# Kernel optimization log

Measured on AMD Instinct MI355X. Metric: run time of the kernel, lower is better.

The kernel has to match this reference:

```python
import jax, jax.numpy as jnp
import numpy as np

N_FFT = 1024
HOP = 256
BATCH = 16
SAMPLES = 262144


def hann_window(n):
    # torch.hann_window default (periodic=True): 0.5 * (1 - cos(2*pi*k/n))
    k = jnp.arange(n, dtype=jnp.float32)
    return 0.5 - 0.5 * jnp.cos(2.0 * jnp.pi * k / n)


def setup_inputs() -> dict:
    key = jax.random.key(0)
    x = jax.random.normal(key, (BATCH, SAMPLES), dtype=jnp.float32)
    window = hann_window(N_FFT)  # (n_fft,)
    return {"x": x, "window": window}


def reference(x, window):
    # Faithful STFT.forward: pad -> frame (identity-kernel conv1d == gather) ->
    # window -> rfft along the frame axis; norm=None.
    pad = N_FFT - HOP
    pad_left = pad // 2
    xp = jnp.pad(x, ((0, 0), (pad_left, pad - pad_left)))
    n_frames = (xp.shape[1] - N_FFT) // HOP + 1
    # gather-based framing, equivalent to conv1d with eye(n_fft) kernel, stride=hop
    idx = jnp.arange(n_frames)[:, None] * HOP + jnp.arange(N_FFT)[None, :]  # (frames, n_fft)
    frames = xp[:, idx]                       # (B, frames, n_fft)
    frames = frames * window[None, None, :]   # windowing
    spec = jnp.fft.rfft(frames, axis=-1)      # (B, frames, n_bins)
    real = jnp.transpose(spec.real, (0, 2, 1))  # (B, n_bins, frames)
    imag = jnp.transpose(spec.imag, (0, 2, 1))
    return real, imag
```

## Files before the change

kernel.cpp:

```cpp
#include <hip/hip_runtime.h>

#define HOP      256
#define SAMPLES  262144
#define NBINS    513
#define NFRAMES  1024
#define FPB      16

__device__ __forceinline__ float2 cmul(float2 a, float2 b) {
  return make_float2(a.x * b.x - a.y * b.y, a.x * b.y + a.y * b.x);
}
__device__ __forceinline__ float2 lds_ld(const float2* p, int bo) {
  return *(const float2*)((const char*)p + bo);
}
__device__ __forceinline__ void lds_st(float2* p, int bo, float2 v) {
  *(float2*)((char*)p + bo) = v;
}
__device__ __forceinline__ int swz(int c) {
  int H = c >> 6, M = (c >> 3) & 7, L = c & 7;
  return (H << 6) | ((M ^ (H & 1)) << 3) | (L ^ M);
}

__device__ __forceinline__ void fft8(float2 v[8]) {
  const float R = 0.70710678118654752440f;
  float2 s0 = make_float2(v[0].x + v[4].x, v[0].y + v[4].y);
  float2 d0 = make_float2(v[0].x - v[4].x, v[0].y - v[4].y);
  float2 s1 = make_float2(v[1].x + v[5].x, v[1].y + v[5].y);
  float2 d1 = make_float2(v[1].x - v[5].x, v[1].y - v[5].y);
  float2 s2 = make_float2(v[2].x + v[6].x, v[2].y + v[6].y);
  float2 d2 = make_float2(v[2].x - v[6].x, v[2].y - v[6].y);
  float2 s3 = make_float2(v[3].x + v[7].x, v[3].y + v[7].y);
  float2 d3 = make_float2(v[3].x - v[7].x, v[3].y - v[7].y);
  float2 e1 = make_float2(R * (d1.x + d1.y), R * (d1.y - d1.x));
  float2 e2 = make_float2(d2.y, -d2.x);
  float2 e3 = make_float2(R * (d3.y - d3.x), R * (-d3.x - d3.y));
  float2 p0 = make_float2(s0.x + s2.x, s0.y + s2.y);
  float2 q0 = make_float2(s0.x - s2.x, s0.y - s2.y);
  float2 p1 = make_float2(s1.x + s3.x, s1.y + s3.y);
  float2 q1 = make_float2(s1.x - s3.x, s1.y - s3.y);
  float2 q1t = make_float2(q1.y, -q1.x);
  float2 p2 = make_float2(d0.x + e2.x, d0.y + e2.y);
  float2 q2 = make_float2(d0.x - e2.x, d0.y - e2.y);
  float2 p3 = make_float2(e1.x + e3.x, e1.y + e3.y);
  float2 q3 = make_float2(e1.x - e3.x, e1.y - e3.y);
  float2 q3t = make_float2(q3.y, -q3.x);
  v[0] = make_float2(p0.x + p1.x, p0.y + p1.y);
  v[4] = make_float2(p0.x - p1.x, p0.y - p1.y);
  v[2] = make_float2(q0.x + q1t.x, q0.y + q1t.y);
  v[6] = make_float2(q0.x - q1t.x, q0.y - q1t.y);
  v[1] = make_float2(p2.x + p3.x, p2.y + p3.y);
  v[5] = make_float2(p2.x - p3.x, p2.y - p3.y);
  v[3] = make_float2(q2.x + q3t.x, q2.y + q3t.y);
  v[7] = make_float2(q2.x - q3t.x, q2.y - q3t.y);
}

#define UNPK(ZP, KEY, SK, SM, TW, R1, I1, R2, I2) {                  \
    float2 Zk = lds_ld(ZP, ((SK) ^ (KEY)) << 3);                     \
    float2 Zm = lds_ld(ZP, ((SM) ^ (KEY)) << 3);                     \
    float xer  = 0.5f * (Zk.x + Zm.x);                               \
    float xei  = 0.5f * (Zk.y - Zm.y);                               \
    float xo_r = 0.5f * (Zk.y + Zm.y);                               \
    float xo_i = -0.5f * (Zk.x - Zm.x);                              \
    float ur = (TW).x * xo_r - (TW).y * xo_i;                        \
    float ui = (TW).x * xo_i + (TW).y * xo_r;                        \
    R1 = xer + ur; I1 = xei + ui; R2 = xer - ur; I2 = ui - xei; }

__global__ __launch_bounds__(1024, 8)
void stft_kernel(const float* __restrict__ x, const float* __restrict__ win,
                 float* __restrict__ out) {
  __shared__ float2 z[FPB * 512];
  const int t  = threadIdx.x;
  const int b  = blockIdx.x >> 6;
  const int f0 = (blockIdx.x & 63) * FPB;

  {
    const int w = t >> 6;
    const int u = t & 63;
    const int g = u >> 3, m2l = u & 7;
    float2* zf = z + (w << 9);

    const int A0    = (g << 3) | (m2l ^ g);
    const int B1w_e = (A0 ^ w) << 3;
    const int B1w_o = B1w_e ^ 64;
    const int C1    = (g << 6) | ((g & 1) << 3) | m2l;
    const int B1r   = (C1 ^ w) << 3;
    const int D0    = (g << 6) | ((m2l ^ (g & 1)) << 3) | m2l;
    const int B2r   = (D0 ^ w) << 3;
    const int F0    = (m2l << 3) | (g ^ m2l);
    const int B3_e  = (F0 ^ w) << 3;
    const int B3_o  = B3_e ^ 64;

    const float* xb = x + (size_t)b * SAMPLES;
    const int fr   = f0 + w;
    const int base = fr * HOP - 384;
    float2 r[8];
    if (f0 != 0 && f0 != (NFRAMES - FPB)) {
      const float2* xc = (const float2*)(xb + base);
      const float2* wc = (const float2*)win;
#pragma unroll
      for (int n1 = 0; n1 < 8; ++n1) {
        float2 xv = xc[(n1 << 6) + u];
        float2 wv = wc[(n1 << 6) + u];
        r[n1] = make_float2(xv.x * wv.x, xv.y * wv.y);
      }
    } else {
#pragma unroll
      for (int n1 = 0; n1 < 8; ++n1) {
        int s = (n1 << 7) + 2 * u;
        int idx = base + s;
        float2 xv = make_float2(0.f, 0.f);
        if (idx >= 0 && idx < SAMPLES) xv = *(const float2*)(xb + idx);
        float2 wv = *(const float2*)(win + s);
        r[n1] = make_float2(xv.x * wv.x, xv.y * wv.y);
      }
    }

    fft8(r);
    float sn, cs;
    __sincosf((float)u * (-6.28318530717958647693f / 512.f), &sn, &cs);
    {
      float2 w1 = make_float2(cs, sn);
      float2 w2 = cmul(w1, w1);
      float2 w3 = cmul(w2, w1);
      float2 w4 = cmul(w2, w2);
      r[1] = cmul(r[1], w1);
      r[2] = cmul(r[2], w2);
      r[3] = cmul(r[3], w3);
      r[4] = cmul(r[4], w4);
      r[5] = cmul(r[5], cmul(w4, w1));
      r[6] = cmul(r[6], cmul(w4, w2));
      r[7] = cmul(r[7], cmul(w4, w3));
    }
    lds_st(zf, B1w_e,        r[0]);
    lds_st(zf, B1w_o +  512, r[1]);
    lds_st(zf, B1w_e + 1024, r[2]);
    lds_st(zf, B1w_o + 1536, r[3]);
    lds_st(zf, B1w_e + 2048, r[4]);
    lds_st(zf, B1w_o + 2560, r[5]);
    lds_st(zf, B1w_e + 3072, r[6]);
    lds_st(zf, B1w_o + 3584, r[7]);

    float2 y[8];
#pragma unroll
    for (int m1 = 0; m1 < 8; ++m1) y[m1] = lds_ld(zf, B1r ^ (72 * m1));

    fft8(y);
    __sincosf((float)m2l * (-6.28318530717958647693f / 64.f), &sn, &cs);
    {
      float2 w1 = make_float2(cs, sn);
      float2 w2 = cmul(w1, w1);
      float2 w3 = cmul(w2, w1);
      float2 w4 = cmul(w2, w2);
      y[1] = cmul(y[1], w1);
      y[2] = cmul(y[2], w2);
      y[3] = cmul(y[3], w3);
      y[4] = cmul(y[4], w4);
      y[5] = cmul(y[5], cmul(w4, w1));
      y[6] = cmul(y[6], cmul(w4, w2));
      y[7] = cmul(y[7], cmul(w4, w3));
    }
#pragma unroll
    for (int j1 = 0; j1 < 8; ++j1) lds_st(zf, B1r ^ (72 * j1), y[j1]);

    float2 h[8];
#pragma unroll
    for (int m = 0; m < 8; ++m) h[m] = lds_ld(zf, B2r ^ (m << 3));

    fft8(h);
    lds_st(zf, B3_e,        h[0]);
    lds_st(zf, B3_o +  512, h[1]);
    lds_st(zf, B3_e + 1024, h[2]);
    lds_st(zf, B3_o + 1536, h[3]);
    lds_st(zf, B3_e + 2048, h[4]);
    lds_st(zf, B3_o + 2560, h[5]);
    lds_st(zf, B3_e + 3072, h[6]);
    lds_st(zf, B3_o + 3584, h[7]);
  }
  __syncthreads();

  {
    const int f2i = t & 7;
    const int q   = t >> 3;
    const int f   = f2i << 1;
    const int fr  = f0 + f;
    const float2* zp0 = z + (f << 9);
    const float2* zp1 = z + ((f + 1) << 9);

    const int sk0 = swz(q);
    const int sm0 = swz((512 - q) & 511);
    const int sk1 = sk0 + 128;
    const int sm1 = (q == 0) ? 384 : (sm0 - 128);

    float sn, cs;
    __sincosf((float)q * (-6.28318530717958647693f / 1024.f), &sn, &cs);
    const float2 tw0 = make_float2(cs, sn);
    const float2 tw1 = cmul(tw0, make_float2(0.70710678118654752440f,
                                             -0.70710678118654752440f));
    float* out_r = out;
    float* out_i = out + (size_t)16 * NBINS * NFRAMES;
    const size_t o1 = ((size_t)b * NBINS + q) * NFRAMES + fr;
    const size_t o2 = ((size_t)b * NBINS + (512 - q)) * NFRAMES + fr;
    const size_t STP = (size_t)128 * NFRAMES;

    {
      float r1a, i1a, r2a, i2a, r1b, i1b, r2b, i2b;
      UNPK(zp0, f,     sk0, sm0, tw0, r1a, i1a, r2a, i2a)
      UNPK(zp1, f + 1, sk0, sm0, tw0, r1b, i1b, r2b, i2b)
      *(float2*)(out_r + o1) = make_float2(r1a, r1b);
      *(float2*)(out_i + o1) = make_float2(i1a, i1b);
      *(float2*)(out_r + o2) = make_float2(r2a, r2b);
      *(float2*)(out_i + o2) = make_float2(i2a, i2b);
    }
    {
      float r1a, i1a, r2a, i2a, r1b, i1b, r2b, i2b;
      UNPK(zp0, f,     sk1, sm1, tw1, r1a, i1a, r2a, i2a)
      UNPK(zp1, f + 1, sk1, sm1, tw1, r1b, i1b, r2b, i2b)
      *(float2*)(out_r + o1 + STP) = make_float2(r1a, r1b);
      *(float2*)(out_i + o1 + STP) = make_float2(i1a, i1b);
      *(float2*)(out_r + o2 - STP) = make_float2(r2a, r2b);
      *(float2*)(out_i + o2 - STP) = make_float2(i2a, i2b);
    }
    if (q == 0) {
      float2 Za = lds_ld(zp0, (256 ^ f) << 3);
      float2 Zb = lds_ld(zp1, (256 ^ (f + 1)) << 3);
      const size_t o6 = ((size_t)b * NBINS + 256) * NFRAMES + fr;
      *(float2*)(out_r + o6) = make_float2(Za.x, Zb.x);
      *(float2*)(out_i + o6) = make_float2(-Za.y, -Zb.y);
    }
  }
}

extern "C" void kernel_launch(void* const* d_in, const int* in_sizes, int n_in,
                              void* d_out, int out_size, void* d_ws, size_t ws_size,
                              hipStream_t stream) {
  const float* x = (const float*)d_in[0];
  const float* w = (const float*)d_in[1];
  float* out = (float*)d_out;
  (void)in_sizes; (void)n_in; (void)out_size; (void)d_ws; (void)ws_size;
  stft_kernel<<<dim3(1024), dim3(1024), 0, stream>>>(x, w, out);
}
```

Before: 24.41 us.

## Halve block size and process two frames per thread in STFT kernel

Each block now runs 512 threads instead of 1024, and every 64-thread group computes two FFT frames (w and w+8) with interleaved stages. The twiddle factors and window loads are shared across both frames, and the unpack phase loops over two quarter-ranges per thread. The aim is more instruction-level parallelism and less repeated setup per frame. In exchange, register pressure rises and there are fewer threads to hide latency.

```diff
diff --git a/kernel.cpp b/kernel.cpp
--- a/kernel.cpp
+++ b/kernel.cpp
@@ -53,6 +53,48 @@
   v[7] = make_float2(q2.x - q3t.x, q2.y - q3t.y);
 }
 
+#define FFT_S1(R, ZF, E1, O1) {                                          \
+    fft8(R);                                                             \
+    R[1] = cmul(R[1], s1w1);  R[2] = cmul(R[2], s1w2);                   \
+    R[3] = cmul(R[3], s1w3);  R[4] = cmul(R[4], s1w4);                   \
+    R[5] = cmul(R[5], s1w5);  R[6] = cmul(R[6], s1w6);                   \
+    R[7] = cmul(R[7], s1w7);                                             \
+    lds_st(ZF, (E1),        R[0]);                                       \
+    lds_st(ZF, (O1) +  512, R[1]);                                       \
+    lds_st(ZF, (E1) + 1024, R[2]);                                       \
+    lds_st(ZF, (O1) + 1536, R[3]);                                       \
+    lds_st(ZF, (E1) + 2048, R[4]);                                       \
+    lds_st(ZF, (O1) + 2560, R[5]);                                       \
+    lds_st(ZF, (E1) + 3072, R[6]);                                       \
+    lds_st(ZF, (O1) + 3584, R[7]);                                       \
+  }
+
+#define FFT_S2(Y, ZF, BR) {                                              \
+    _Pragma("unroll")                                                    \
+    for (int m1 = 0; m1 < 8; ++m1) Y[m1] = lds_ld(ZF, (BR) ^ (72 * m1)); \
+    fft8(Y);                                                             \
+    Y[1] = cmul(Y[1], s2w1);  Y[2] = cmul(Y[2], s2w2);                   \
+    Y[3] = cmul(Y[3], s2w3);  Y[4] = cmul(Y[4], s2w4);                   \
+    Y[5] = cmul(Y[5], s2w5);  Y[6] = cmul(Y[6], s2w6);                   \
+    Y[7] = cmul(Y[7], s2w7);                                             \
+    _Pragma("unroll")                                                    \
+    for (int j1 = 0; j1 < 8; ++j1) lds_st(ZF, (BR) ^ (72 * j1), Y[j1]);  \
+  }
+
+#define FFT_S3(H, ZF, B2, E3, O3) {                                      \
+    _Pragma("unroll")                                                    \
+    for (int m = 0; m < 8; ++m) H[m] = lds_ld(ZF, (B2) ^ (m << 3));      \
+    fft8(H);                                                             \
+    lds_st(ZF, (E3),        H[0]);                                       \
+    lds_st(ZF, (O3) +  512, H[1]);                                       \
+    lds_st(ZF, (E3) + 1024, H[2]);                                       \
+    lds_st(ZF, (O3) + 1536, H[3]);                                       \
+    lds_st(ZF, (E3) + 2048, H[4]);                                       \
+    lds_st(ZF, (O3) + 2560, H[5]);                                       \
+    lds_st(ZF, (E3) + 3072, H[6]);                                       \
+    lds_st(ZF, (O3) + 3584, H[7]);                                       \
+  }
+
 #define UNPK(ZP, KEY, SK, SM, TW, R1, I1, R2, I2) {                  \
     float2 Zk = lds_ld(ZP, ((SK) ^ (KEY)) << 3);                     \
     float2 Zm = lds_ld(ZP, ((SM) ^ (KEY)) << 3);                     \
@@ -64,7 +106,7 @@
     float ui = (TW).x * xo_i + (TW).y * xo_r;                        \
     R1 = xer + ur; I1 = xei + ui; R2 = xer - ur; I2 = ui - xei; }
 
-__global__ __launch_bounds__(1024, 8)
+__global__ __launch_bounds__(512, 4)
 void stft_kernel(const float* __restrict__ x, const float* __restrict__ win,
                  float* __restrict__ out) {
   __shared__ float2 z[FPB * 512];
@@ -76,7 +118,8 @@
     const int w = t >> 6;
     const int u = t & 63;
     const int g = u >> 3, m2l = u & 7;
-    float2* zf = z + (w << 9);
+    float2* zfA = z + (w << 9);
+    float2* zfB = z + ((w + 8) << 9);
 
     const int A0    = (g << 3) | (m2l ^ g);
     const int B1w_e = (A0 ^ w) << 3;
@@ -90,90 +133,74 @@
     const int B3_o  = B3_e ^ 64;
 
     const float* xb = x + (size_t)b * SAMPLES;
-    const int fr   = f0 + w;
-    const int base = fr * HOP - 384;
-    float2 r[8];
-    if (f0 != 0 && f0 != (NFRAMES - FPB)) {
-      const float2* xc = (const float2*)(xb + base);
-      const float2* wc = (const float2*)win;
+    const int baseA = (f0 + w) * HOP - 384;
+    const int baseB = baseA + 8 * HOP;
+    const float2* wc = (const float2*)win;
+    float2 ra[8], rb[8];
+    if (f0 != 0) {
+      const float2* xc = (const float2*)(xb + baseA);
+#pragma unroll
+      for (int n1 = 0; n1 < 8; ++n1) ra[n1] = xc[(n1 << 6) + u];
+    } else {
 #pragma unroll
       for (int n1 = 0; n1 < 8; ++n1) {
-        float2 xv = xc[(n1 << 6) + u];
-        float2 wv = wc[(n1 << 6) + u];
-        r[n1] = make_float2(xv.x * wv.x, xv.y * wv.y);
-      }
+        int idx = baseA + (n1 << 7) + 2 * u;
+        ra[n1] = make_float2(0.f, 0.f);
+        if (idx >= 0) ra[n1] = *(const float2*)(xb + idx);
+      }
+    }
+    if (f0 != (NFRAMES - FPB)) {
+      const float2* xc = (const float2*)(xb + baseB);
+#pragma unroll
+      for (int n1 = 0; n1 < 8; ++n1) rb[n1] = xc[(n1 << 6) + u];
     } else {
 #pragma unroll
       for (int n1 = 0; n1 < 8; ++n1) {
-        int s = (n1 << 7) + 2 * u;
-        int idx = base + s;
-        float2 xv = make_float2(0.f, 0.f);
-        if (idx >= 0 && idx < SAMPLES) xv = *(const float2*)(xb + idx);
-        float2 wv = *(const float2*)(win + s);
-        r[n1] = make_float2(xv.x * wv.x, xv.y * wv.y);
-      }
-    }
-
-    fft8(r);
+        int idx = baseB + (n1 << 7) + 2 * u;
+        rb[n1] = make_float2(0.f, 0.f);
+        if (idx < SAMPLES) rb[n1] = *(const float2*)(xb + idx);
+      }
+    }
+
     float sn, cs;
     __sincosf((float)u * (-6.28318530717958647693f / 512.f), &sn, &cs);
+    const float2 s1w1 = make_float2(cs, sn);
+    const float2 s1w2 = cmul(s1w1, s1w1);
+    const float2 s1w3 = cmul(s1w2, s1w1);
+    const float2 s1w4 = cmul(s1w2, s1w2);
+    const float2 s1w5 = cmul(s1w4, s1w1);
+    const float2 s1w6 = cmul(s1w4, s1w2);
+    const float2 s1w7 = cmul(s1w4, s1w3);
+    __sincosf((float)m2l * (-6.28318530717958647693f / 64.f), &sn, &cs);
+    const float2 s2w1 = make_float2(cs, sn);
+    const float2 s2w2 = cmul(s2w1, s2w1);
+    const float2 s2w3 = cmul(s2w2, s2w1);
+    const float2 s2w4 = cmul(s2w2, s2w2);
+    const float2 s2w5 = cmul(s2w4, s2w1);
+    const float2 s2w6 = cmul(s2w4, s2w2);
+    const float2 s2w7 = cmul(s2w4, s2w3);
+
+#pragma unroll
+    for (int n1 = 0; n1 < 8; ++n1) {
+      float2 wv = wc[(n1 << 6) + u];
+      ra[n1] = make_float2(ra[n1].x * wv.x, ra[n1].y * wv.y);
+      rb[n1] = make_float2(rb[n1].x * wv.x, rb[n1].y * wv.y);
+    }
+
+    FFT_S1(ra, zfA, B1w_e, B1w_o)
+    FFT_S1(rb, zfB, B1w_o, B1w_e)
     {
-      float2 w1 = make_float2(cs, sn);
-      float2 w2 = cmul(w1, w1);
-      float2 w3 = cmul(w2, w1);
-      float2 w4 = cmul(w2, w2);
-      r[1] = cmul(r[1], w1);
-      r[2] = cmul(r[2], w2);
-      r[3] = cmul(r[3], w3);
-      r[4] = cmul(r[4], w4);
-      r[5] = cmul(r[5], cmul(w4, w1));
-      r[6] = cmul(r[6], cmul(w4, w2));
-      r[7] = cmul(r[7], cmul(w4, w3));
-    }
-    lds_st(zf, B1w_e,        r[0]);
-    lds_st(zf, B1w_o +  512, r[1]);
-    lds_st(zf, B1w_e + 1024, r[2]);
-    lds_st(zf, B1w_o + 1536, r[3]);
-    lds_st(zf, B1w_e + 2048, r[4]);
-    lds_st(zf, B1w_o + 2560, r[5]);
-    lds_st(zf, B1w_e + 3072, r[6]);
-    lds_st(zf, B1w_o + 3584, r[7]);
-
-    float2 y[8];
-#pragma unroll
-    for (int m1 = 0; m1 < 8; ++m1) y[m1] = lds_ld(zf, B1r ^ (72 * m1));
-
-    fft8(y);
-    __sincosf((float)m2l * (-6.28318530717958647693f / 64.f), &sn, &cs);
+      float2 y[8];
+      FFT_S2(y, zfA, B1r)
+      float2 y2[8];
+      FFT_S2(y2, zfB, B1r ^ 64)
+    }
     {
-      float2 w1 = make_float2(cs, sn);
-      float2 w2 = cmul(w1, w1);
-      float2 w3 = cmul(w2, w1);
-      float2 w4 = cmul(w2, w2);
-      y[1] = cmul(y[1], w1);
-      y[2] = cmul(y[2], w2);
-      y[3] = cmul(y[3], w3);
-      y[4] = cmul(y[4], w4);
-      y[5] = cmul(y[5], cmul(w4, w1));
-      y[6] = cmul(y[6], cmul(w4, w2));
-      y[7] = cmul(y[7], cmul(w4, w3));
-    }
-#pragma unroll
-    for (int j1 = 0; j1 < 8; ++j1) lds_st(zf, B1r ^ (72 * j1), y[j1]);
-
-    float2 h[8];
-#pragma unroll
-    for (int m = 0; m < 8; ++m) h[m] = lds_ld(zf, B2r ^ (m << 3));
-
-    fft8(h);
-    lds_st(zf, B3_e,        h[0]);
-    lds_st(zf, B3_o +  512, h[1]);
-    lds_st(zf, B3_e + 1024, h[2]);
-    lds_st(zf, B3_o + 1536, h[3]);
-    lds_st(zf, B3_e + 2048, h[4]);
-    lds_st(zf, B3_o + 2560, h[5]);
-    lds_st(zf, B3_e + 3072, h[6]);
-    lds_st(zf, B3_o + 3584, h[7]);
+      float2 h[8];
+      FFT_S3(h, zfA, B2r, B3_e, B3_o)
+      float2 h2[8];
+      FFT_S3(h2, zfB, B2r ^ 64, B3_o, B3_e)
+    }
   }
   __syncthreads();
 
@@ -184,40 +211,47 @@
     const int fr  = f0 + f;
     const float2* zp0 = z + (f << 9);
     const float2* zp1 = z + ((f + 1) << 9);
-
-    const int sk0 = swz(q);
-    const int sm0 = swz((512 - q) & 511);
-    const int sk1 = sk0 + 128;
-    const int sm1 = (q == 0) ? 384 : (sm0 - 128);
+    float* out_r = out;
+    float* out_i = out + (size_t)16 * NBINS * NFRAMES;
+    const size_t STP = (size_t)128 * NFRAMES;
 
     float sn, cs;
     __sincosf((float)q * (-6.28318530717958647693f / 1024.f), &sn, &cs);
-    const float2 tw0 = make_float2(cs, sn);
-    const float2 tw1 = cmul(tw0, make_float2(0.70710678118654752440f,
-                                             -0.70710678118654752440f));
-    float* out_r = out;
-    float* out_i = out + (size_t)16 * NBINS * NFRAMES;
-    const size_t o1 = ((size_t)b * NBINS + q) * NFRAMES + fr;
-    const size_t o2 = ((size_t)b * NBINS + (512 - q)) * NFRAMES + fr;
-    const size_t STP = (size_t)128 * NFRAMES;
-
-    {
-      float r1a, i1a, r2a, i2a, r1b, i1b, r2b, i2b;
-      UNPK(zp0, f,     sk0, sm0, tw0, r1a, i1a, r2a, i2a)
-      UNPK(zp1, f + 1, sk0, sm0, tw0, r1b, i1b, r2b, i2b)
-      *(float2*)(out_r + o1) = make_float2(r1a, r1b);
-      *(float2*)(out_i + o1) = make_float2(i1a, i1b);
-      *(float2*)(out_r + o2) = make_float2(r2a, r2b);
-      *(float2*)(out_i + o2) = make_float2(i2a, i2b);
-    }
-    {
-      float r1a, i1a, r2a, i2a, r1b, i1b, r2b, i2b;
-      UNPK(zp0, f,     sk1, sm1, tw1, r1a, i1a, r2a, i2a)
-      UNPK(zp1, f + 1, sk1, sm1, tw1, r1b, i1b, r2b, i2b)
-      *(float2*)(out_r + o1 + STP) = make_float2(r1a, r1b);
-      *(float2*)(out_i + o1 + STP) = make_float2(i1a, i1b);
-      *(float2*)(out_r + o2 - STP) = make_float2(r2a, r2b);
-      *(float2*)(out_i + o2 - STP) = make_float2(i2a, i2b);
+    const float2 twq = make_float2(cs, sn);
+
+#pragma unroll
+    for (int hh = 0; hh < 2; ++hh) {
+      const int qq  = q + (hh << 6);
+      const int sk0 = swz(qq);
+      const int sm0 = swz((512 - qq) & 511);
+      const int sk1 = sk0 + 128;
+      const int sm1 = (qq == 0) ? 384 : (sm0 - 128);
+      const float2 tw0 = hh ? cmul(twq, make_float2(0.92387953251128675613f,
+                                                    -0.38268343236508977173f))
+                            : twq;
+      const float2 tw1 = cmul(tw0, make_float2(0.70710678118654752440f,
+                                               -0.70710678118654752440f));
+      const size_t o1 = ((size_t)b * NBINS + qq) * NFRAMES + fr;
+      const size_t o2 = ((size_t)b * NBINS + (512 - qq)) * NFRAMES + fr;
+
+      {
+        float r1a, i1a, r2a, i2a, r1b, i1b, r2b, i2b;
+        UNPK(zp0, f,     sk0, sm0, tw0, r1a, i1a, r2a, i2a)
+        UNPK(zp1, f + 1, sk0, sm0, tw0, r1b, i1b, r2b, i2b)
+        *(float2*)(out_r + o1) = make_float2(r1a, r1b);
+        *(float2*)(out_i + o1) = make_float2(i1a, i1b);
+        *(float2*)(out_r + o2) = make_float2(r2a, r2b);
+        *(float2*)(out_i + o2) = make_float2(i2a, i2b);
+      }
+      {
+        float r1a, i1a, r2a, i2a, r1b, i1b, r2b, i2b;
+        UNPK(zp0, f,     sk1, sm1, tw1, r1a, i1a, r2a, i2a)
+        UNPK(zp1, f + 1, sk1, sm1, tw1, r1b, i1b, r2b, i2b)
+        *(float2*)(out_r + o1 + STP) = make_float2(r1a, r1b);
+        *(float2*)(out_i + o1 + STP) = make_float2(i1a, i1b);
+        *(float2*)(out_r + o2 - STP) = make_float2(r2a, r2b);
+        *(float2*)(out_i + o2 - STP) = make_float2(i2a, i2b);
+      }
     }
     if (q == 0) {
       float2 Za = lds_ld(zp0, (256 ^ f) << 3);
@@ -236,5 +270,5 @@
   const float* w = (const float*)d_in[1];
   float* out = (float*)d_out;
   (void)in_sizes; (void)n_in; (void)out_size; (void)d_ws; (void)ws_size;
-  stft_kernel<<<dim3(1024), dim3(1024), 0, stream>>>(x, w, out);
-}
+  stft_kernel<<<dim3(1024), dim3(512), 0, stream>>>(x, w, out);
+}
```

New measurement: 24.85 us. About the same (+1.8%).

## Precompute FFT twiddles and half-scaled window in LDS tables

Applied to the files above, without the earlier changes.

Twiddle factors for the two radix-8 stages and the real-FFT unpack step are now computed once per block into shared-memory tables instead of being derived per thread through sincos and chained complex multiplies. The window is staged in LDS pre-scaled by 0.5, which removes the 0.5 factors from the unpack arithmetic, and the Nyquist-bin output is doubled to match. Global loads of x are issued before the table setup so their latency overlaps it. The cost is an extra block barrier and more LDS per block, which may reduce occupancy.

```diff
diff --git a/kernel.cpp b/kernel.cpp
--- a/kernel.cpp
+++ b/kernel.cpp
@@ -56,10 +56,10 @@
 #define UNPK(ZP, KEY, SK, SM, TW, R1, I1, R2, I2) {                  \
     float2 Zk = lds_ld(ZP, ((SK) ^ (KEY)) << 3);                     \
     float2 Zm = lds_ld(ZP, ((SM) ^ (KEY)) << 3);                     \
-    float xer  = 0.5f * (Zk.x + Zm.x);                               \
-    float xei  = 0.5f * (Zk.y - Zm.y);                               \
-    float xo_r = 0.5f * (Zk.y + Zm.y);                               \
-    float xo_i = -0.5f * (Zk.x - Zm.x);                              \
+    float xer  = Zk.x + Zm.x;                                        \
+    float xei  = Zk.y - Zm.y;                                        \
+    float xo_r = Zk.y + Zm.y;                                        \
+    float xo_i = Zm.x - Zk.x;                                        \
     float ur = (TW).x * xo_r - (TW).y * xo_i;                        \
     float ui = (TW).x * xo_i + (TW).y * xo_r;                        \
     R1 = xer + ur; I1 = xei + ui; R2 = xer - ur; I2 = ui - xei; }
@@ -68,16 +68,57 @@
 void stft_kernel(const float* __restrict__ x, const float* __restrict__ win,
                  float* __restrict__ out) {
   __shared__ float2 z[FPB * 512];
+  __shared__ float2 T1[7][64];
+  __shared__ float2 T2[7][8];
+  __shared__ float2 TU[256];
+  __shared__ float  WH[1024];
+
   const int t  = threadIdx.x;
   const int b  = blockIdx.x >> 6;
   const int f0 = (blockIdx.x & 63) * FPB;
+  const int w  = t >> 6;
+  const int u  = t & 63;
+  const int g  = u >> 3, m2l = u & 7;
+
+  const float* xb = x + (size_t)b * SAMPLES;
+  const int base = (f0 + w) * HOP - 384;
+  float2 r[8];
+  if (f0 != 0 && f0 != (NFRAMES - FPB)) {
+    const float2* xc = (const float2*)(xb + base);
+#pragma unroll
+    for (int n1 = 0; n1 < 8; ++n1) r[n1] = xc[(n1 << 6) + u];
+  } else {
+#pragma unroll
+    for (int n1 = 0; n1 < 8; ++n1) {
+      int idx = base + (n1 << 7) + 2 * u;
+      r[n1] = make_float2(0.f, 0.f);
+      if (idx >= 0 && idx < SAMPLES) r[n1] = *(const float2*)(xb + idx);
+    }
+  }
 
   {
-    const int w = t >> 6;
-    const int u = t & 63;
-    const int g = u >> 3, m2l = u & 7;
+    WH[t] = 0.5f * win[t];
+    float sn, cs;
+    if (t < 448) {
+      int k = t >> 6, uu = t & 63;
+      __sincosf((float)(uu * (k + 1)) * (-6.28318530717958647693f / 512.f),
+                &sn, &cs);
+      T1[k][uu] = make_float2(cs, sn);
+    } else if (t < 504) {
+      int i = t - 448, k = i >> 3, m = i & 7;
+      __sincosf((float)(m * (k + 1)) * (-6.28318530717958647693f / 64.f),
+                &sn, &cs);
+      T2[k][m] = make_float2(cs, sn);
+    } else if (t >= 512 && t < 768) {
+      int kk = t - 512;
+      __sincosf((float)kk * (-6.28318530717958647693f / 1024.f), &sn, &cs);
+      TU[kk] = make_float2(cs, sn);
+    }
+  }
+  __syncthreads();
+
+  {
     float2* zf = z + (w << 9);
-
     const int A0    = (g << 3) | (m2l ^ g);
     const int B1w_e = (A0 ^ w) << 3;
     const int B1w_o = B1w_e ^ 64;
@@ -89,47 +130,16 @@
     const int B3_e  = (F0 ^ w) << 3;
     const int B3_o  = B3_e ^ 64;
 
-    const float* xb = x + (size_t)b * SAMPLES;
-    const int fr   = f0 + w;
-    const int base = fr * HOP - 384;
-    float2 r[8];
-    if (f0 != 0 && f0 != (NFRAMES - FPB)) {
-      const float2* xc = (const float2*)(xb + base);
-      const float2* wc = (const float2*)win;
-#pragma unroll
-      for (int n1 = 0; n1 < 8; ++n1) {
-        float2 xv = xc[(n1 << 6) + u];
-        float2 wv = wc[(n1 << 6) + u];
-        r[n1] = make_float2(xv.x * wv.x, xv.y * wv.y);
-      }
-    } else {
-#pragma unroll
-      for (int n1 = 0; n1 < 8; ++n1) {
-        int s = (n1 << 7) + 2 * u;
-        int idx = base + s;
-        float2 xv = make_float2(0.f, 0.f);
-        if (idx >= 0 && idx < SAMPLES) xv = *(const float2*)(xb + idx);
-        float2 wv = *(const float2*)(win + s);
-        r[n1] = make_float2(xv.x * wv.x, xv.y * wv.y);
-      }
+    const float2* wh2 = (const float2*)WH;
+#pragma unroll
+    for (int n1 = 0; n1 < 8; ++n1) {
+      float2 wv = wh2[(n1 << 6) + u];
+      r[n1] = make_float2(r[n1].x * wv.x, r[n1].y * wv.y);
     }
 
     fft8(r);
-    float sn, cs;
-    __sincosf((float)u * (-6.28318530717958647693f / 512.f), &sn, &cs);
-    {
-      float2 w1 = make_float2(cs, sn);
-      float2 w2 = cmul(w1, w1);
-      float2 w3 = cmul(w2, w1);
-      float2 w4 = cmul(w2, w2);
-      r[1] = cmul(r[1], w1);
-      r[2] = cmul(r[2], w2);
-      r[3] = cmul(r[3], w3);
-      r[4] = cmul(r[4], w4);
-      r[5] = cmul(r[5], cmul(w4, w1));
-      r[6] = cmul(r[6], cmul(w4, w2));
-      r[7] = cmul(r[7], cmul(w4, w3));
-    }
+#pragma unroll
+    for (int k = 1; k < 8; ++k) r[k] = cmul(r[k], T1[k - 1][u]);
     lds_st(zf, B1w_e,        r[0]);
     lds_st(zf, B1w_o +  512, r[1]);
     lds_st(zf, B1w_e + 1024, r[2]);
@@ -144,20 +154,8 @@
     for (int m1 = 0; m1 < 8; ++m1) y[m1] = lds_ld(zf, B1r ^ (72 * m1));
 
     fft8(y);
-    __sincosf((float)m2l * (-6.28318530717958647693f / 64.f), &sn, &cs);
-    {
-      float2 w1 = make_float2(cs, sn);
-      float2 w2 = cmul(w1, w1);
-      float2 w3 = cmul(w2, w1);
-      float2 w4 = cmul(w2, w2);
-      y[1] = cmul(y[1], w1);
-      y[2] = cmul(y[2], w2);
-      y[3] = cmul(y[3], w3);
-      y[4] = cmul(y[4], w4);
-      y[5] = cmul(y[5], cmul(w4, w1));
-      y[6] = cmul(y[6], cmul(w4, w2));
-      y[7] = cmul(y[7], cmul(w4, w3));
-    }
+#pragma unroll
+    for (int k = 1; k < 8; ++k) y[k] = cmul(y[k], T2[k - 1][m2l]);
 #pragma unroll
     for (int j1 = 0; j1 < 8; ++j1) lds_st(zf, B1r ^ (72 * j1), y[j1]);
 
@@ -190,11 +188,8 @@
     const int sk1 = sk0 + 128;
     const int sm1 = (q == 0) ? 384 : (sm0 - 128);
 
-    float sn, cs;
-    __sincosf((float)q * (-6.28318530717958647693f / 1024.f), &sn, &cs);
-    const float2 tw0 = make_float2(cs, sn);
-    const float2 tw1 = cmul(tw0, make_float2(0.70710678118654752440f,
-                                             -0.70710678118654752440f));
+    const float2 tw0 = TU[q];
+    const float2 tw1 = TU[q + 128];
     float* out_r = out;
     float* out_i = out + (size_t)16 * NBINS * NFRAMES;
     const size_t o1 = ((size_t)b * NBINS + q) * NFRAMES + fr;
@@ -223,8 +218,8 @@
       float2 Za = lds_ld(zp0, (256 ^ f) << 3);
       float2 Zb = lds_ld(zp1, (256 ^ (f + 1)) << 3);
       const size_t o6 = ((size_t)b * NBINS + 256) * NFRAMES + fr;
-      *(float2*)(out_r + o6) = make_float2(Za.x, Zb.x);
-      *(float2*)(out_i + o6) = make_float2(-Za.y, -Zb.y);
+      *(float2*)(out_r + o6) = make_float2(Za.x + Za.x, Zb.x + Zb.x);
+      *(float2*)(out_i + o6) = make_float2(-(Za.y + Za.y), -(Zb.y + Zb.y));
     }
   }
 }
```

Result: faster. 23.92 us (-2.0%).
